# Kernel optimization log

Hardware: AMD Instinct MI355X
Metric: run time of the kernel (lower is better)

Reference implementation:

```python
import jax, jax.numpy as jnp
import numpy as np

STATE_DIM = 2048
OBS_DIM = 512
STEPS = 8192
PROC_STD = 0.1 ** 0.5   # sqrt(process_noise_var)
OBS_STD = 0.5 ** 0.5    # sqrt(observation_noise_var)


def setup_inputs() -> dict:
    key = jax.random.key(0)
    k1, k2, k3, k4, k5 = jax.random.split(key, 5)
    initial_state = jax.random.normal(k1, (STATE_DIM,), dtype=jnp.float32)
    process_noise = jax.random.normal(k2, (STEPS, STATE_DIM), dtype=jnp.float32)
    obs_noise = jax.random.normal(k3, (STEPS, OBS_DIM), dtype=jnp.float32)
    # Near-stable transition matrix (torch default is exactly identity, which is
    # marginally stable; keep spectral radius < 1 for an 8192-step rollout).
    A = 0.99 * jnp.eye(STATE_DIM, dtype=jnp.float32) \
        + 1e-4 * jax.random.normal(k4, (STATE_DIM, STATE_DIM), dtype=jnp.float32)
    C = 0.02 * jax.random.normal(k5, (OBS_DIM, STATE_DIM), dtype=jnp.float32)
    return {
        "initial_state": initial_state,
        "A": A,
        "C": C,
        "process_noise": process_noise,
        "obs_noise": obs_noise,
        "steps": STEPS,
    }


def reference(initial_state, A, C, process_noise, obs_noise, steps):
    # obs_t   = C @ state_t + obs_noise_t   * sqrt(obs_var)
    # state_{t+1} = A @ state_t + proc_noise_t * sqrt(proc_var)
    def step(state, noises):
        pn, on = noises
        obs = C @ state + on * OBS_STD
        new_state = A @ state + pn * PROC_STD
        return new_state, obs

    _, observations = jax.lax.scan(step, initial_state, (process_noise, obs_noise))
    return observations  # (steps, obs_dim)
```

## Files before the change

### kernel.cpp

```cpp
#include <hip/hip_runtime.h>


#define SD 2048
#define OD 512
#define NT 8192
#define BLK 64
#define KB 128
#define KBP (KB+16)
#define NP 7
#define NPH 6
#define NPN 5
#define PROC_STD 0.31622776601683794f
#define OBS_STD  0.7071067811865476f

typedef __attribute__((ext_vector_type(8))) short v8s;
typedef __attribute__((ext_vector_type(4))) float v4f;

__device__ __forceinline__ unsigned short f2bf(float f) {
    union { float f; unsigned int u; } v; v.f = f;
    unsigned int r = v.u + 0x7fffu + ((v.u >> 16) & 1u);
    return (unsigned short)(r >> 16);
}
__device__ __forceinline__ float bf2f(unsigned short u) {
    union { unsigned int ui; float f; } cv; cv.ui = (unsigned int)u << 16;
    return cv.f;
}

#define GLD16(g, l) __builtin_amdgcn_global_load_lds( \
    (const __attribute__((address_space(1))) unsigned int*)(g), \
    (__attribute__((address_space(3))) unsigned int*)(l), 16, 0, 0)


__device__ __forceinline__ void body_g64(unsigned short* SH,
        const unsigned short* __restrict__ A,
        const unsigned short* __restrict__ B, int ldb,
        int tM, int tN, int mode,
        unsigned short* __restrict__ obf, int ldo,
        float* __restrict__ o32,
        const unsigned short* __restrict__ X1,
        const unsigned short* __restrict__ X2,
        float c1, float c2) {
    unsigned short* Al = SH;
    unsigned short* Xt = SH + 64 * 40;
    int tid = threadIdx.x, lane = tid & 63, w = tid >> 6;
    int m16 = lane & 15, q = lane >> 4;
    int ar = tid >> 2, ao = (tid & 3) * 8;
    int xk = tid >> 3, xn = (tid & 7) * 8;
    int qb = xk >> 3;
    v4f acc[4] = {{0,0,0,0},{0,0,0,0},{0,0,0,0},{0,0,0,0}};

    v8s av = *(const v8s*)(A + (size_t)(tM + ar) * SD + ao);
    v8s xv = *(const v8s*)(B + (size_t)xk * ldb + tN + xn);
    for (int k0 = 0; k0 < SD; k0 += 32) {
        *(v8s*)(Al + ar * 40 + ao) = av;
#pragma unroll
        for (int c = 0; c < 8; ++c) {
            int n = xn + c, sw = (n >> 3) & 3;
            Xt[n * 40 + (((qb ^ sw) << 3) | (xk & 7))] = xv[c];
        }
        __syncthreads();
        if (k0 + 32 < SD) {
            av = *(const v8s*)(A + (size_t)(tM + ar) * SD + (k0 + 32) + ao);
            xv = *(const v8s*)(B + (size_t)(k0 + 32 + xk) * ldb + tN + xn);
        }
        v8s a = *(const v8s*)(Al + (w * 16 + m16) * 40 + q * 8);
#pragma unroll
        for (int c = 0; c < 4; ++c) {
            int nl = c * 16 + m16, swn = (nl >> 3) & 3;
            v8s b = *(const v8s*)(Xt + nl * 40 + ((q ^ swn) << 3));
            acc[c] = __builtin_amdgcn_mfma_f32_16x16x32_bf16(a, b, acc[c], 0, 0, 0);
        }
        __syncthreads();
    }
#pragma unroll
    for (int c = 0; c < 4; ++c)
#pragma unroll
        for (int j = 0; j < 4; ++j) {
            int r = tM + w * 16 + q * 4 + j;
            int col = tN + c * 16 + m16;
            float v = acc[c][j];
            if (mode == 2) {
                size_t iS = (size_t)r * SD + col;
                v += o32[iS] + c1 * bf2f(X1[iS]) + c2 * bf2f(X2[iS]);
                o32[iS] = v;
                obf[iS] = f2bf(v);
            } else if (mode == 3) {
                size_t iS = (size_t)r * SD + col;
                v = c1 * o32[iS] + v;
                o32[iS] = v;
                obf[iS] = f2bf(v);
            } else if (mode == 1) {
                o32[(size_t)r * ldo + col] = v;
            } else {
                obf[(size_t)r * ldo + col] = f2bf(v);
            }
        }
}

__device__ __forceinline__ void body_horner(unsigned short* SH, int bx,
        const unsigned short* __restrict__ Abf,
        const unsigned short* __restrict__ Xbf,
        const float* __restrict__ Wp,
        float* __restrict__ X32o,
        unsigned short* __restrict__ Xbfo) {
    unsigned short* Al = SH;
    unsigned short* Xt = SH + 32 * 72;
    int tM = (bx & 63) * 32, tN = (bx >> 6) * 32;
    int tid = threadIdx.x, lane = tid & 63, w = tid >> 6;
    int m16 = lane & 15, q = lane >> 4;
    int ar = tid >> 3, ao = (tid & 7) * 8;
    int xk = tid >> 2, xn = (tid & 3) * 8;
    int qb = xk >> 3;
    v4f acc = {0, 0, 0, 0};
    v8s av = *(const v8s*)(Abf + (size_t)(tM + ar) * SD + ao);
    v8s xv = *(const v8s*)(Xbf + (size_t)xk * KB + tN + xn);
    int nl = (w & 1) * 16 + m16;
    int swn = (nl >> 3) & 3;
    int rl = (w >> 1) * 16 + m16;
    for (int k0 = 0; k0 < SD; k0 += 64) {
        *(v8s*)(Al + ar * 72 + ao) = av;
#pragma unroll
        for (int c = 0; c < 8; ++c) {
            int n = xn + c, sw = (n >> 3) & 3;
            Xt[n * 72 + (((qb ^ sw) << 3) | (xk & 7))] = xv[c];
        }
        __syncthreads();
        if (k0 + 64 < SD) {
            av = *(const v8s*)(Abf + (size_t)(tM + ar) * SD + (k0 + 64) + ao);
            xv = *(const v8s*)(Xbf + (size_t)(k0 + 64 + xk) * KB + tN + xn);
        }
#pragma unroll
        for (int ch = 0; ch < 2; ++ch) {
            v8s a = *(const v8s*)(Al + rl * 72 + ch * 32 + q * 8);
            int q2 = ch * 4 + q;
            v8s b = *(const v8s*)(Xt + nl * 72 + ((q2 ^ swn) << 3));
            acc = __builtin_amdgcn_mfma_f32_16x16x32_bf16(a, b, acc, 0, 0, 0);
        }
        __syncthreads();
    }
#pragma unroll
    for (int j = 0; j < 4; ++j) {
        int r = tM + (w >> 1) * 16 + q * 4 + j;
        int kc = tN + (w & 1) * 16 + m16;
        int idx = r * KB + kc;
        float v = acc[j] + Wp[idx];
        X32o[idx] = v;
        if (Xbfo) Xbfo[idx] = f2bf(v);
    }
}

__device__ __forceinline__ void body_scan(unsigned short* SH, int bx,
        const unsigned short* __restrict__ Mrbf,
        const unsigned short* __restrict__ Sbf_in,
        const float* __restrict__ S32_in,
        float* __restrict__ S32_out,
        unsigned short* __restrict__ Sbf_out,
        float ar, int shift) {
    unsigned short* Al = SH;
    unsigned short* Xt = SH + 32 * 72;
    int tM = (bx & 63) * 32, tN = (bx >> 6) * 32;
    int tid = threadIdx.x, lane = tid & 63, w = tid >> 6;
    int m16 = lane & 15, q = lane >> 4;
    int ar_ = tid >> 3, ao = (tid & 7) * 8;
    int xk = tid >> 2, xn = (tid & 3) * 8;
    int qb = xk >> 3;
    int coff = tN + xn + 16 - shift;
    v4f acc = {0, 0, 0, 0};
    v8s av = *(const v8s*)(Mrbf + (size_t)(tM + ar_) * SD + ao);
    v8s xv = *(const v8s*)(Sbf_in + (size_t)xk * KBP + coff);
    int nl = (w & 1) * 16 + m16;
    int swn = (nl >> 3) & 3;
    int rl = (w >> 1) * 16 + m16;
    for (int k0 = 0; k0 < SD; k0 += 64) {
        *(v8s*)(Al + ar_ * 72 + ao) = av;
#pragma unroll
        for (int c = 0; c < 8; ++c) {
            int n = xn + c, sw = (n >> 3) & 3;
            Xt[n * 72 + (((qb ^ sw) << 3) | (xk & 7))] = xv[c];
        }
        __syncthreads();
        if (k0 + 64 < SD) {
            av = *(const v8s*)(Mrbf + (size_t)(tM + ar_) * SD + (k0 + 64) + ao);
            xv = *(const v8s*)(Sbf_in + (size_t)(k0 + 64 + xk) * KBP + coff);
        }
#pragma unroll
        for (int ch = 0; ch < 2; ++ch) {
            v8s a = *(const v8s*)(Al + rl * 72 + ch * 32 + q * 8);
            int q2 = ch * 4 + q;
            v8s b = *(const v8s*)(Xt + nl * 72 + ((q2 ^ swn) << 3));
            acc = __builtin_amdgcn_mfma_f32_16x16x32_bf16(a, b, acc, 0, 0, 0);
        }
        __syncthreads();
    }
#pragma unroll
    for (int j = 0; j < 4; ++j) {
        int r = tM + (w >> 1) * 16 + q * 4 + j;
        int kc = tN + (w & 1) * 16 + m16;
        int idx = r * KB + kc;
        int ksh = kc - shift;
        float v = S32_in[idx] + acc[j] + (ksh >= 0 ? ar * S32_in[r * KB + ksh] : 0.f);
        S32_out[idx] = v;
        Sbf_out[(size_t)r * KBP + kc + 16] = f2bf(v);
    }
}

__device__ __forceinline__ void body_g128(unsigned short* SH, int bid,
        const unsigned short* __restrict__ Aptr, int lda,
        const unsigned short* __restrict__ Bptr, int ldb,
        int mtiles, int npx,
        unsigned short* __restrict__ obf, size_t ldo) {
    unsigned short* As = SH;
    unsigned short* Bs = SH + 4096;
    int tid = threadIdx.x, lane = tid & 63, w = tid >> 6;
    int mT = (bid >> 3) % mtiles;
    int nT = (bid & 7) * npx + (bid >> 3) / mtiles;
    int tM = mT * 128, tN = nT * 128;
    int wr = w >> 1, wc = w & 1;
    int m16 = lane & 15, q = lane >> 4;
    int srow = lane >> 2, sk8 = lane & 3;
    const unsigned short* ga0 = Aptr + (size_t)(tM + w * 16 + srow) * lda + sk8 * 8;
    const unsigned short* ga1 = ga0 + (size_t)64 * lda;
    const unsigned short* gb0 = Bptr + (size_t)(tN + w * 16 + srow) * ldb + sk8 * 8;
    const unsigned short* gb1 = gb0 + (size_t)64 * ldb;
    unsigned short* la0 = As + w * 512;
    unsigned short* la1 = As + 2048 + w * 512;
    unsigned short* lb0 = Bs + w * 512;
    unsigned short* lb1 = Bs + 2048 + w * 512;

    v4f acc[4][4];
#pragma unroll
    for (int mi = 0; mi < 4; ++mi)
#pragma unroll
        for (int ni = 0; ni < 4; ++ni) acc[mi][ni] = (v4f){0, 0, 0, 0};

    GLD16(ga0, la0); GLD16(ga1, la1); GLD16(gb0, lb0); GLD16(gb1, lb1);
    ga0 += 32; ga1 += 32; gb0 += 32; gb1 += 32;
    __syncthreads();

    int arow = (wr * 64 + m16) * 32 + q * 8;
    int brow = (wc * 64 + m16) * 32 + q * 8;
    for (int k0 = 0; k0 < SD; k0 += 32) {
        v8s a[4], b[4];
#pragma unroll
        for (int mi = 0; mi < 4; ++mi) a[mi] = *(const v8s*)(As + arow + mi * 512);
#pragma unroll
        for (int ni = 0; ni < 4; ++ni) b[ni] = *(const v8s*)(Bs + brow + ni * 512);
        __syncthreads();
        if (k0 + 32 < SD) {
            GLD16(ga0, la0); GLD16(ga1, la1); GLD16(gb0, lb0); GLD16(gb1, lb1);
            ga0 += 32; ga1 += 32; gb0 += 32; gb1 += 32;
        }
#pragma unroll
        for (int mi = 0; mi < 4; ++mi)
#pragma unroll
            for (int ni = 0; ni < 4; ++ni)
                acc[mi][ni] = __builtin_amdgcn_mfma_f32_16x16x32_bf16(a[mi], b[ni],
                                                                      acc[mi][ni], 0, 0, 0);
        __syncthreads();
    }
#pragma unroll
    for (int mi = 0; mi < 4; ++mi)
#pragma unroll
        for (int ni = 0; ni < 4; ++ni)
#pragma unroll
            for (int j = 0; j < 4; ++j) {
                int row = tM + wr * 64 + mi * 16 + q * 4 + j;
                int col = tN + wc * 64 + ni * 16 + m16;
                obf[(size_t)row * ldo + col] = f2bf(acc[mi][ni][j]);
            }
}


__device__ double d_binom(int m, int p) {
    if (p < 0 || p > m) return 0.0;
    double c = 1.0;
    for (int q = 1; q <= p; ++q) c = c * (double)(m - p + q) / (double)q;
    return c;
}
__device__ double d_p99(int n) {
    double r = 1.0;
    for (int q = 0; q < n; ++q) r *= 0.99;
    return r;
}

__global__ __launch_bounds__(256) void k_prepAll(const float* __restrict__ A,
                                                 const float* __restrict__ C,
                                                 unsigned short* __restrict__ Ebf,
                                                 float* __restrict__ M, float c1,
                                                 unsigned short* __restrict__ Cbf,
                                                 float* __restrict__ wW,
                                                 float* __restrict__ cW,
                                                 unsigned short* __restrict__ Tbf) {
    int bid = blockIdx.x;
    if (bid < 16384) {
        int idx = bid * 256 + threadIdx.x;
        int r = idx >> 11, c = idx & 2047;
        float e = A[idx] - (r == c ? 0.99f : 0.0f);
        Ebf[idx] = f2bf(e);
        M[idx] = c1 * e;
    } else if (bid < 20480) {
        int idx = (bid - 16384) * 256 + threadIdx.x;
        Cbf[idx] = f2bf(C[idx]);
    } else {
        int idx = (bid - 20480) * 256 + threadIdx.x;
        if (idx < NP * 64) {
            int p = idx >> 6, j = idx & 63;
            int m = 63 - j;
            wW[idx] = (p <= m) ? (float)((double)PROC_STD * d_binom(m, p) * d_p99(m - p)) : 0.f;
            cW[idx] = (p <= j) ? (float)(d_binom(j, p) * d_p99(j - p)) : 0.f;
        }
        if (idx < NP * 64 * 64) {
            int p = idx >> 12, j = (idx >> 6) & 63, i = idx & 63;
            int mm = i - 1 - j;
            float t = (mm >= p) ? (float)((double)PROC_STD * d_binom(mm, p) * d_p99(mm - p)) : 0.f;
            Tbf[idx] = f2bf(t);
        }
    }
}

__global__ __launch_bounds__(256) void k_wsum(const float* __restrict__ pn,
                                              const float* __restrict__ wW,
                                              float* __restrict__ W32,
                                              unsigned short* __restrict__ Wbf,
                                              unsigned short* __restrict__ Vbf,
                                              unsigned short* __restrict__ pnbf) {
    __shared__ float ws[NP * 64];
    int tid = threadIdx.x;
    for (int t = tid; t < NP * 64; t += 256) ws[t] = wW[t];
    __syncthreads();
    int bx = blockIdx.x;
    int k = bx >> 1, dc = bx & 1;
    int d0 = dc * 1024 + tid * 4;
    float acc[NP][4];
#pragma unroll
    for (int p = 0; p < NP; ++p)
#pragma unroll
        for (int u = 0; u < 4; ++u) acc[p][u] = 0.f;
    for (int j = 0; j < 64; ++j) {
        size_t gi = (size_t)(k * BLK + j) * SD + d0;
        float4 v = *(const float4*)(pn + gi);
        ushort4 b4;
        b4.x = f2bf(v.x); b4.y = f2bf(v.y); b4.z = f2bf(v.z); b4.w = f2bf(v.w);
        *(ushort4*)(pnbf + gi) = b4;
#pragma unroll
        for (int p = 0; p < NP; ++p) {
            float wv = ws[p * 64 + j];
            acc[p][0] += wv * v.x; acc[p][1] += wv * v.y;
            acc[p][2] += wv * v.z; acc[p][3] += wv * v.w;
        }
    }
#pragma unroll
    for (int jj = 0; jj < 3; ++jj)
#pragma unroll
        for (int u = 0; u < 4; ++u) {
            W32[((size_t)jj * SD + d0 + u) * KB + k] = acc[2 * jj][u];
            Wbf[((size_t)jj * SD + d0 + u) * KB + k] = f2bf(acc[2 * jj + 1][u]);
        }
#pragma unroll
    for (int u = 0; u < 4; ++u)
        Vbf[(size_t)(d0 + u) * KB + k] = f2bf(acc[6][u]);
}

__global__ __launch_bounds__(256) void k_combP(const unsigned short* __restrict__ Ebf,
                                               const unsigned short* __restrict__ E2,
                                               const unsigned short* __restrict__ E3,
                                               unsigned short* __restrict__ P,
                                               float c4, float c5, float c6) {
    int idx = blockIdx.x * 256 + threadIdx.x;
    P[idx] = f2bf(c4 * bf2f(Ebf[idx]) + c5 * bf2f(E2[idx]) + c6 * bf2f(E3[idx]));
}

__global__ __launch_bounds__(256) void k_nn_ce(const unsigned short* __restrict__ L,
                                               const unsigned short* __restrict__ X,
                                               unsigned short* __restrict__ NNout,
                                               const unsigned short* __restrict__ CEa,
                                               const unsigned short* __restrict__ CEb,
                                               unsigned short* __restrict__ CEout) {
    __shared__ __align__(16) unsigned short SH[5120];
    int bid = blockIdx.x;
    if (bid < 1024)
        body_g64(SH, L, X, SD, (bid & 31) * 64, (bid >> 5) * 64, 0, NNout, SD,
                 nullptr, nullptr, nullptr, 0.f, 0.f);
    else {
        int bx = bid - 1024;
        body_g64(SH, CEa, CEb, SD, (bx & 7) * 64, (bx >> 3) * 64, 0, CEout, SD,
                 nullptr, nullptr, nullptr, 0.f, 0.f);
    }
}

__global__ __launch_bounds__(256) void k_M_Y(const unsigned short* __restrict__ E3,
                                             const unsigned short* __restrict__ P,
                                             float* __restrict__ M32,
                                             const unsigned short* __restrict__ E2,
                                             unsigned short* __restrict__ Mbf,
                                             float c2, float c3,
                                             const unsigned short* __restrict__ Ebf,
                                             const unsigned short* __restrict__ Wbf,
                                             const float* __restrict__ W32,
                                             float* __restrict__ Y32) {
    __shared__ __align__(16) unsigned short SH[5120];
    int bid = blockIdx.x;
    if (bid < 1024)
        body_g64(SH, E3, P, SD, (bid & 31) * 64, (bid >> 5) * 64, 2, Mbf, SD,
                 M32, E2, E3, c2, c3);
    else {
        int l = bid - 1024;
        int j = l >> 8, bx = l & 255;
        body_horner(SH, bx, Ebf, Wbf + (size_t)j * SD * KB, W32 + (size_t)j * SD * KB,
                    Y32 + (size_t)j * SD * KB, nullptr);
    }
}

__global__ __launch_bounds__(256) void k_ce2_z(const unsigned short* __restrict__ CEall,
                                               const unsigned short* __restrict__ E2,
                                               const float* __restrict__ Y32,
                                               const unsigned short* __restrict__ Vbf0,
                                               float* __restrict__ V32o,
                                               unsigned short* __restrict__ Vbfo) {
    __shared__ __align__(16) unsigned short SH[5120];
    int bid = blockIdx.x;
    if (bid < 512) {
        int y = bid >> 8, bx = bid & 255;
        body_g64(SH, CEall + (size_t)(1 + y) * OD * SD, E2, SD,
                 (bx & 7) * 64, (bx >> 3) * 64, 0,
                 (unsigned short*)(CEall + (size_t)(3 + y) * OD * SD), SD,
                 nullptr, nullptr, nullptr, 0.f, 0.f);
    } else
        body_horner(SH, bid - 512, E2, Vbf0, Y32 + (size_t)2 * SD * KB, V32o, Vbfo);
}

__global__ __launch_bounds__(256) void k_ce1_z(const unsigned short* __restrict__ CEall,
                                               const unsigned short* __restrict__ E2,
                                               const float* __restrict__ Y32,
                                               const unsigned short* __restrict__ Vbf1,
                                               float* __restrict__ V32o,
                                               unsigned short* __restrict__ Vbfo) {
    __shared__ __align__(16) unsigned short SH[5120];
    int bid = blockIdx.x;
    if (bid < 256)
        body_g64(SH, CEall + (size_t)3 * OD * SD, E2, SD,
                 (bid & 7) * 64, (bid >> 3) * 64, 0,
                 (unsigned short*)(CEall + (size_t)5 * OD * SD), SD,
                 nullptr, nullptr, nullptr, 0.f, 0.f);
    else
        body_horner(SH, bid - 256, E2, Vbf1, Y32 + (size_t)SD * KB, V32o, Vbfo);
}

__global__ __launch_bounds__(256) void k_hornerZ(const unsigned short* __restrict__ E2,
                                                 const unsigned short* __restrict__ Vbf0,
                                                 const float* __restrict__ Y32,
                                                 float* __restrict__ V32o) {
    __shared__ __align__(16) unsigned short SH[5120];
    body_horner(SH, blockIdx.x, E2, Vbf0, Y32, V32o, nullptr);
}

__global__ __launch_bounds__(256) void k_scan_init(const float* __restrict__ s0,
                                                   const float* __restrict__ U,
                                                   float* __restrict__ S32,
                                                   unsigned short* __restrict__ Sbf0,
                                                   unsigned short* __restrict__ Sbf1) {
    int idx = blockIdx.x * 256 + threadIdx.x;
    int d = idx / KBP, c = idx - d * KBP;
    if (c < 16) { Sbf0[idx] = 0; Sbf1[idx] = 0; return; }
    int k = c - 16;
    float v = (k == 0) ? s0[d] : U[(size_t)d * KB + (k - 1)];
    S32[(size_t)d * KB + k] = v;
    Sbf0[idx] = f2bf(v);
}

__global__ __launch_bounds__(256) void k_sqscan(const unsigned short* __restrict__ Lbf,
                                                float* __restrict__ M32,
                                                unsigned short* __restrict__ Mbfo,
                                                float twoa,
                                                const unsigned short* __restrict__ Sbf_in,
                                                const float* __restrict__ S32_in,
                                                float* __restrict__ S32_out,
                                                unsigned short* __restrict__ Sbf_out,
                                                float ar, int shift) {
    __shared__ __align__(16) unsigned short SH[5120];
    int bid = blockIdx.x;
    if (bid < 1024)
        body_g64(SH, Lbf, Lbf, SD, (bid & 31) * 64, (bid >> 5) * 64, 3, Mbfo, SD,
                 M32, nullptr, nullptr, twoa, 0.f);
    else
        body_scan(SH, bid - 1024, Lbf, Sbf_in, S32_in, S32_out, Sbf_out, ar, shift);
}

__global__ __launch_bounds__(256) void k_scan3(const unsigned short* __restrict__ Mrbf,
                                               const unsigned short* __restrict__ Sbf_in,
                                               const float* __restrict__ S32_in,
                                               float* __restrict__ S32_out,
                                               unsigned short* __restrict__ Sbf_out,
                                               float ar, int shift) {
    __shared__ __align__(16) unsigned short SH[5120];
    body_scan(SH, blockIdx.x, Mrbf, Sbf_in, S32_in, S32_out, Sbf_out, ar, shift);
}

__global__ __launch_bounds__(256) void k_scan16(const float* __restrict__ S32_in,
                                                float* __restrict__ S32_out,
                                                unsigned short* __restrict__ Sbf_out,
                                                float a4) {
    int idx = blockIdx.x * 256 + threadIdx.x;
    int d = idx >> 7, k = idx & 127;
    float v = S32_in[idx] + (k >= 16 ? a4 * S32_in[idx - 16] : 0.f);
    S32_out[idx] = v;
    Sbf_out[(size_t)d * KBP + k + 16] = f2bf(v);
}

__global__ __launch_bounds__(256) void k_pall_h(const unsigned short* __restrict__ CEall,
                                                const unsigned short* __restrict__ pnbf,
                                                unsigned short* __restrict__ Pall,
                                                const unsigned short* __restrict__ Sbf16,
                                                float* __restrict__ H) {
    __shared__ __align__(16) unsigned short SH[8192];
    int bid = blockIdx.x;
    if (bid < 1280)
        body_g128(SH, bid, CEall, SD, pnbf, SD, 20, 8, Pall, (size_t)NT);
    else {
        int l = bid - 1280;
        int y = l >> 4, bx = l & 15;
        body_g64(SH, CEall + (size_t)y * OD * SD, Sbf16, KBP,
                 (bx & 7) * 64, (bx >> 3) * 64, 1, nullptr, KB,
                 H + (size_t)y * OD * KB, nullptr, nullptr, 0.f, 0.f);
    }
}

__global__ __launch_bounds__(256) void k_final2(const unsigned short* __restrict__ P,
                                                const unsigned short* __restrict__ Tbf,
                                                const float* __restrict__ H,
                                                const float* __restrict__ cW,
                                                const float* __restrict__ on,
                                                float* __restrict__ out) {
    __shared__ __align__(16) float obsT[64][65];
    unsigned short* Al = (unsigned short*)obsT;
    unsigned short* Xt = Al + 64 * 40;
    int bx = blockIdx.x;
    int kb = bx >> 3, ob = bx & 7;
    int o0 = ob * 64;
    int tid = threadIdx.x, lane = tid & 63, w = tid >> 6;
    int m16 = lane & 15, q = lane >> 4;
    int ar = tid >> 2, ao = (tid & 3) * 8;
    int xk = tid >> 3, xn = (tid & 7) * 8;
    int qb = xk >> 3;
    v4f acc[4] = {{0,0,0,0},{0,0,0,0},{0,0,0,0},{0,0,0,0}};
    const unsigned short* Abase = P + (size_t)kb * 64;

    v8s av = *(const v8s*)(Abase + (size_t)(o0 + ar) * NT + ao);
    v8s xv = *(const v8s*)(Tbf + xk * 64 + xn);
    for (int kc = 0; kc < 2 * NPN; ++kc) {
        *(v8s*)(Al + ar * 40 + ao) = av;
#pragma unroll
        for (int c = 0; c < 8; ++c) {
            int n = xn + c, sw = (n >> 3) & 3;
            Xt[n * 40 + (((qb ^ sw) << 3) | (xk & 7))] = xv[c];
        }
        __syncthreads();
        if (kc + 1 < 2 * NPN) {
            int p = (kc + 1) >> 1, j0 = ((kc + 1) & 1) * 32;
            av = *(const v8s*)(Abase + (size_t)(p * OD + o0 + ar) * NT + j0 + ao);
            xv = *(const v8s*)(Tbf + p * 4096 + (j0 + xk) * 64 + xn);
        }
        v8s a = *(const v8s*)(Al + (w * 16 + m16) * 40 + q * 8);
#pragma unroll
        for (int c = 0; c < 4; ++c) {
            int nl = c * 16 + m16, swn = (nl >> 3) & 3;
            v8s b = *(const v8s*)(Xt + nl * 40 + ((q ^ swn) << 3));
            acc[c] = __builtin_amdgcn_mfma_f32_16x16x32_bf16(a, b, acc[c], 0, 0, 0);
        }
        __syncthreads();
    }
#pragma unroll
    for (int c = 0; c < 4; ++c)
#pragma unroll
        for (int j = 0; j < 4; ++j)
            obsT[w * 16 + q * 4 + j][c * 16 + m16] = acc[c][j];
    __syncthreads();
    int g = tid >> 6;
    float Hv[NPH];
#pragma unroll
    for (int p = 0; p < NPH; ++p)
        Hv[p] = H[((size_t)p * OD + o0 + lane) * KB + kb];
#pragma unroll
    for (int r = 0; r < 16; ++r) {
        int trow = r * 4 + g;
        float a2 = obsT[lane][trow];
#pragma unroll
        for (int p = 0; p < NPH; ++p) a2 += cW[p * 64 + trow] * Hv[p];
        size_t oidx = (size_t)(kb * 64 + trow) * OD + o0 + lane;
        out[oidx] = a2 + OBS_STD * on[oidx];
    }
}

extern "C" void kernel_launch(void* const* d_in, const int* in_sizes, int n_in,
                              void* d_out, int out_size, void* d_ws, size_t ws_size,
                              hipStream_t stream) {
    const float* s0 = (const float*)d_in[0];
    const float* A  = (const float*)d_in[1];
    const float* C  = (const float*)d_in[2];
    const float* pn = (const float*)d_in[3];
    const float* on = (const float*)d_in[4];
    float* out = (float*)d_out;

    char* p = (char*)d_ws;
    auto take = [&](size_t n) { char* r = p; p += (n + 255) & ~(size_t)255; return r; };
    unsigned short* Ebf = (unsigned short*)take((size_t)SD * SD * 2);
    unsigned short* CEall = (unsigned short*)take((size_t)NPH * OD * SD * 2);
    float* M            = (float*)take((size_t)SD * SD * 4);
    unsigned short* Xp0 = (unsigned short*)take((size_t)SD * SD * 2);
    unsigned short* Xp1 = (unsigned short*)take((size_t)SD * SD * 2);
    unsigned short* Xp2 = (unsigned short*)take((size_t)SD * SD * 2);
    unsigned short* Pall = (unsigned short*)M;
    unsigned short* Mbf = (unsigned short*)take((size_t)SD * SD * 2);
    float* W32          = (float*)take((size_t)3 * SD * KB * 4);
    unsigned short* Wbf = (unsigned short*)take((size_t)3 * SD * KB * 2);
    float* Y32          = (float*)take((size_t)3 * SD * KB * 4);
    float* V32[2] = {(float*)take((size_t)SD * KB * 4), (float*)take((size_t)SD * KB * 4)};
    unsigned short* Vbf[2] = {(unsigned short*)take((size_t)SD * KB * 2),
                              (unsigned short*)take((size_t)SD * KB * 2)};
    float* SC32[2] = {(float*)take((size_t)SD * KB * 4), (float*)take((size_t)SD * KB * 4)};
    unsigned short* SCbf[2] = {(unsigned short*)take((size_t)SD * KBP * 2),
                               (unsigned short*)take((size_t)SD * KBP * 2)};
    float* wW   = (float*)take((size_t)NP * 64 * 4);
    float* cW   = (float*)take((size_t)NP * 64 * 4);
    unsigned short* Tbf = (unsigned short*)take((size_t)NP * 64 * 64 * 2);
    unsigned short* pnbf = (unsigned short*)take((size_t)SD * NT * 2);
    float* H    = (float*)take((size_t)NPH * OD * KB * 4);

    double pw[65]; pw[0] = 1.0;
    for (int m = 1; m <= 64; ++m) pw[m] = pw[m - 1] * 0.99;
    const double bin[7] = {1, 64, 2016, 41664, 635376, 7624512, 74974368};
    float cf[7];
    for (int m = 1; m <= 6; ++m) cf[m] = (float)(bin[m] * pw[64 - m]);
    float a64 = (float)pw[64];

    k_prepAll<<<20592, 256, 0, stream>>>(A, C, Ebf, M, cf[1], CEall, wW, cW, Tbf);
    k_wsum<<<256, 256, 0, stream>>>(pn, wW, W32, Wbf, Vbf[0], pnbf);
    k_nn_ce<<<1280, 256, 0, stream>>>(Ebf, Ebf, Xp0, CEall, Ebf, CEall + (size_t)OD * SD);
    k_nn_ce<<<1280, 256, 0, stream>>>(Ebf, Xp0, Xp1, CEall, Xp0, CEall + (size_t)2 * OD * SD);
    k_combP<<<SD * SD / 256, 256, 0, stream>>>(Ebf, Xp0, Xp1, Xp2, cf[4], cf[5], cf[6]);
    k_M_Y<<<1792, 256, 0, stream>>>(Xp1, Xp2, M, Xp0, Mbf, cf[2], cf[3], Ebf, Wbf, W32, Y32);
    k_ce2_z<<<768, 256, 0, stream>>>(CEall, Xp0, Y32, Vbf[0], V32[1], Vbf[1]);
    k_ce1_z<<<512, 256, 0, stream>>>(CEall, Xp0, Y32, Vbf[1], V32[0], Vbf[0]);
    k_hornerZ<<<256, 256, 0, stream>>>(Xp0, Vbf[0], Y32, V32[1]);
    k_scan_init<<<SD * KBP / 256, 256, 0, stream>>>(s0, V32[1], SC32[0], SCbf[0], SCbf[1]);
    float a = a64;
    k_sqscan<<<1280, 256, 0, stream>>>(Mbf, M, Xp0, 2.f * a,
                                       SCbf[0], SC32[0], SC32[1], SCbf[1], a, 1);
    a *= a;
    k_sqscan<<<1280, 256, 0, stream>>>(Xp0, M, Mbf, 2.f * a,
                                       SCbf[1], SC32[1], SC32[0], SCbf[0], a, 2);
    a *= a;
    k_sqscan<<<1280, 256, 0, stream>>>(Mbf, M, Xp0, 2.f * a,
                                       SCbf[0], SC32[0], SC32[1], SCbf[1], a, 4);
    a *= a;
    k_scan3<<<256, 256, 0, stream>>>(Xp0, SCbf[1], SC32[1], SC32[0], SCbf[0], a, 8);
    a *= a;
    k_scan16<<<SD * KB / 256, 256, 0, stream>>>(SC32[0], SC32[1], SCbf[1], a);
    k_pall_h<<<1376, 256, 0, stream>>>(CEall, pnbf, Pall, SCbf[1] + 16, H);
    k_final2<<<1024, 256, 0, stream>>>(Pall, Tbf, H, cW, on, out);
}
```

Baseline: 787.8 us.

## Fuse small elementwise kernels into GEMM epilogues and drop fp32 M copy

Removes the fp32 M matrix: the squaring epilogues now read the bf16 previous operand instead of fp32 state, and k_prepAll no longer writes M. Folds the combP polynomial into the second nn GEMM epilogue (mode 4) and the scan-init into the Horner kernel. Co-schedules the scan3 step with the Pall GEMM and applies the last scan16 shift algebraically inside k_final2 on G. This cuts kernel launches and the memory traffic of several full 2048x2048 passes, at the cost of lower precision in the M recurrence (bf16 instead of fp32 accumulation).

```diff
diff --git a/kernel.cpp b/kernel.cpp
--- a/kernel.cpp
+++ b/kernel.cpp
@@ -39,7 +39,9 @@
         float* __restrict__ o32,
         const unsigned short* __restrict__ X1,
         const unsigned short* __restrict__ X2,
-        float c1, float c2) {
+        const unsigned short* __restrict__ X3,
+        unsigned short* __restrict__ Pout,
+        float c1, float c2, float c3) {
     unsigned short* Al = SH;
     unsigned short* Xt = SH + 64 * 40;
     int tid = threadIdx.x, lane = tid & 63, w = tid >> 6;
@@ -79,16 +81,16 @@
             int r = tM + w * 16 + q * 4 + j;
             int col = tN + c * 16 + m16;
             float v = acc[c][j];
+            size_t iS = (size_t)r * SD + col;
             if (mode == 2) {
-                size_t iS = (size_t)r * SD + col;
-                v += o32[iS] + c1 * bf2f(X1[iS]) + c2 * bf2f(X2[iS]);
-                o32[iS] = v;
+                v += c1 * bf2f(X1[iS]) + c2 * bf2f(X2[iS]) + c3 * bf2f(X3[iS]);
                 obf[iS] = f2bf(v);
             } else if (mode == 3) {
-                size_t iS = (size_t)r * SD + col;
-                v = c1 * o32[iS] + v;
-                o32[iS] = v;
+                v = c1 * bf2f(X1[iS]) + v;
                 obf[iS] = f2bf(v);
+            } else if (mode == 4) {
+                obf[iS] = f2bf(v);
+                Pout[iS] = f2bf(c1 * bf2f(X1[iS]) + c2 * bf2f(X2[iS]) + c3 * v);
             } else if (mode == 1) {
                 o32[(size_t)r * ldo + col] = v;
             } else {
@@ -102,7 +104,8 @@
         const unsigned short* __restrict__ Xbf,
         const float* __restrict__ Wp,
         float* __restrict__ X32o,
-        unsigned short* __restrict__ Xbfo) {
+        unsigned short* __restrict__ Xbfo,
+        int initShift) {
     unsigned short* Al = SH;
     unsigned short* Xt = SH + 32 * 72;
     int tM = (bx & 63) * 32, tN = (bx >> 6) * 32;
@@ -142,10 +145,16 @@
     for (int j = 0; j < 4; ++j) {
         int r = tM + (w >> 1) * 16 + q * 4 + j;
         int kc = tN + (w & 1) * 16 + m16;
-        int idx = r * KB + kc;
-        float v = acc[j] + Wp[idx];
-        X32o[idx] = v;
-        if (Xbfo) Xbfo[idx] = f2bf(v);
+        float v = acc[j] + Wp[r * KB + kc];
+        if (initShift) {
+            if (kc < 127) {
+                X32o[r * KB + kc + 1] = v;
+                Xbfo[(size_t)r * KBP + kc + 17] = f2bf(v);
+            }
+        } else {
+            X32o[r * KB + kc] = v;
+            if (Xbfo) Xbfo[r * KB + kc] = f2bf(v);
+        }
     }
 }
 
@@ -286,7 +295,6 @@
 __global__ __launch_bounds__(256) void k_prepAll(const float* __restrict__ A,
                                                  const float* __restrict__ C,
                                                  unsigned short* __restrict__ Ebf,
-                                                 float* __restrict__ M, float c1,
                                                  unsigned short* __restrict__ Cbf,
                                                  float* __restrict__ wW,
                                                  float* __restrict__ cW,
@@ -297,7 +305,6 @@
         int r = idx >> 11, c = idx & 2047;
         float e = A[idx] - (r == c ? 0.99f : 0.0f);
         Ebf[idx] = f2bf(e);
-        M[idx] = c1 * e;
     } else if (bid < 20480) {
         int idx = (bid - 16384) * 256 + threadIdx.x;
         Cbf[idx] = f2bf(C[idx]);
@@ -361,40 +368,35 @@
         Vbf[(size_t)(d0 + u) * KB + k] = f2bf(acc[6][u]);
 }
 
-__global__ __launch_bounds__(256) void k_combP(const unsigned short* __restrict__ Ebf,
-                                               const unsigned short* __restrict__ E2,
-                                               const unsigned short* __restrict__ E3,
-                                               unsigned short* __restrict__ P,
-                                               float c4, float c5, float c6) {
-    int idx = blockIdx.x * 256 + threadIdx.x;
-    P[idx] = f2bf(c4 * bf2f(Ebf[idx]) + c5 * bf2f(E2[idx]) + c6 * bf2f(E3[idx]));
-}
-
 __global__ __launch_bounds__(256) void k_nn_ce(const unsigned short* __restrict__ L,
                                                const unsigned short* __restrict__ X,
                                                unsigned short* __restrict__ NNout,
                                                const unsigned short* __restrict__ CEa,
                                                const unsigned short* __restrict__ CEb,
-                                               unsigned short* __restrict__ CEout) {
+                                               unsigned short* __restrict__ CEout,
+                                               int mode,
+                                               unsigned short* __restrict__ Pout,
+                                               const unsigned short* __restrict__ X1,
+                                               const unsigned short* __restrict__ X2,
+                                               float c1, float c2, float c3) {
     __shared__ __align__(16) unsigned short SH[5120];
     int bid = blockIdx.x;
     if (bid < 1024)
-        body_g64(SH, L, X, SD, (bid & 31) * 64, (bid >> 5) * 64, 0, NNout, SD,
-                 nullptr, nullptr, nullptr, 0.f, 0.f);
+        body_g64(SH, L, X, SD, (bid & 31) * 64, (bid >> 5) * 64, mode, NNout, SD,
+                 nullptr, X1, X2, nullptr, Pout, c1, c2, c3);
     else {
         int bx = bid - 1024;
         body_g64(SH, CEa, CEb, SD, (bx & 7) * 64, (bx >> 3) * 64, 0, CEout, SD,
-                 nullptr, nullptr, nullptr, 0.f, 0.f);
+                 nullptr, nullptr, nullptr, nullptr, nullptr, 0.f, 0.f, 0.f);
     }
 }
 
 __global__ __launch_bounds__(256) void k_M_Y(const unsigned short* __restrict__ E3,
                                              const unsigned short* __restrict__ P,
-                                             float* __restrict__ M32,
+                                             const unsigned short* __restrict__ Ebf,
                                              const unsigned short* __restrict__ E2,
                                              unsigned short* __restrict__ Mbf,
-                                             float c2, float c3,
-                                             const unsigned short* __restrict__ Ebf,
+                                             float c1, float c2, float c3,
                                              const unsigned short* __restrict__ Wbf,
                                              const float* __restrict__ W32,
                                              float* __restrict__ Y32) {
@@ -402,12 +404,12 @@
     int bid = blockIdx.x;
     if (bid < 1024)
         body_g64(SH, E3, P, SD, (bid & 31) * 64, (bid >> 5) * 64, 2, Mbf, SD,
-                 M32, E2, E3, c2, c3);
+                 nullptr, Ebf, E2, E3, nullptr, c1, c2, c3);
     else {
         int l = bid - 1024;
         int j = l >> 8, bx = l & 255;
         body_horner(SH, bx, Ebf, Wbf + (size_t)j * SD * KB, W32 + (size_t)j * SD * KB,
-                    Y32 + (size_t)j * SD * KB, nullptr);
+                    Y32 + (size_t)j * SD * KB, nullptr, 0);
     }
 }
 
@@ -424,9 +426,9 @@
         body_g64(SH, CEall + (size_t)(1 + y) * OD * SD, E2, SD,
                  (bx & 7) * 64, (bx >> 3) * 64, 0,
                  (unsigned short*)(CEall + (size_t)(3 + y) * OD * SD), SD,
-                 nullptr, nullptr, nullptr, 0.f, 0.f);
+                 nullptr, nullptr, nullptr, nullptr, nullptr, 0.f, 0.f, 0.f);
     } else
-        body_horner(SH, bid - 512, E2, Vbf0, Y32 + (size_t)2 * SD * KB, V32o, Vbfo);
+        body_horner(SH, bid - 512, E2, Vbf0, Y32 + (size_t)2 * SD * KB, V32o, Vbfo, 0);
 }
 
 __global__ __launch_bounds__(256) void k_ce1_z(const unsigned short* __restrict__ CEall,
@@ -441,35 +443,36 @@
         body_g64(SH, CEall + (size_t)3 * OD * SD, E2, SD,
                  (bid & 7) * 64, (bid >> 3) * 64, 0,
                  (unsigned short*)(CEall + (size_t)5 * OD * SD), SD,
-                 nullptr, nullptr, nullptr, 0.f, 0.f);
+                 nullptr, nullptr, nullptr, nullptr, nullptr, 0.f, 0.f, 0.f);
     else
-        body_horner(SH, bid - 256, E2, Vbf1, Y32 + (size_t)SD * KB, V32o, Vbfo);
-}
-
-__global__ __launch_bounds__(256) void k_hornerZ(const unsigned short* __restrict__ E2,
-                                                 const unsigned short* __restrict__ Vbf0,
-                                                 const float* __restrict__ Y32,
-                                                 float* __restrict__ V32o) {
+        body_horner(SH, bid - 256, E2, Vbf1, Y32 + (size_t)SD * KB, V32o, Vbfo, 0);
+}
+
+__global__ __launch_bounds__(256) void k_hornerZI(const unsigned short* __restrict__ E2,
+                                                  const unsigned short* __restrict__ Vbf0,
+                                                  const float* __restrict__ Y32,
+                                                  const float* __restrict__ s0,
+                                                  float* __restrict__ S32,
+                                                  unsigned short* __restrict__ Sbf0,
+                                                  unsigned short* __restrict__ Sbf1) {
     __shared__ __align__(16) unsigned short SH[5120];
-    body_horner(SH, blockIdx.x, E2, Vbf0, Y32, V32o, nullptr);
-}
-
-__global__ __launch_bounds__(256) void k_scan_init(const float* __restrict__ s0,
-                                                   const float* __restrict__ U,
-                                                   float* __restrict__ S32,
-                                                   unsigned short* __restrict__ Sbf0,
-                                                   unsigned short* __restrict__ Sbf1) {
-    int idx = blockIdx.x * 256 + threadIdx.x;
-    int d = idx / KBP, c = idx - d * KBP;
-    if (c < 16) { Sbf0[idx] = 0; Sbf1[idx] = 0; return; }
-    int k = c - 16;
-    float v = (k == 0) ? s0[d] : U[(size_t)d * KB + (k - 1)];
-    S32[(size_t)d * KB + k] = v;
-    Sbf0[idx] = f2bf(v);
+    int bid = blockIdx.x;
+    if (bid < 256)
+        body_horner(SH, bid, E2, Vbf0, Y32, S32, Sbf0, 1);
+    else {
+        int idx = (bid - 256) * 256 + threadIdx.x;
+        int d = idx >> 4, c = idx & 15;
+        Sbf0[(size_t)d * KBP + c] = 0;
+        Sbf1[(size_t)d * KBP + c] = 0;
+        if (c == 0) {
+            float v = s0[d];
+            S32[d * KB] = v;
+            Sbf0[(size_t)d * KBP + 16] = f2bf(v);
+        }
+    }
 }
 
 __global__ __launch_bounds__(256) void k_sqscan(const unsigned short* __restrict__ Lbf,
-                                                float* __restrict__ M32,
                                                 unsigned short* __restrict__ Mbfo,
                                                 float twoa,
                                                 const unsigned short* __restrict__ Sbf_in,
@@ -481,56 +484,45 @@
     int bid = blockIdx.x;
     if (bid < 1024)
         body_g64(SH, Lbf, Lbf, SD, (bid & 31) * 64, (bid >> 5) * 64, 3, Mbfo, SD,
-                 M32, nullptr, nullptr, twoa, 0.f);
+                 nullptr, Lbf, nullptr, nullptr, nullptr, twoa, 0.f, 0.f);
     else
         body_scan(SH, bid - 1024, Lbf, Sbf_in, S32_in, S32_out, Sbf_out, ar, shift);
 }
 
-__global__ __launch_bounds__(256) void k_scan3(const unsigned short* __restrict__ Mrbf,
-                                               const unsigned short* __restrict__ Sbf_in,
-                                               const float* __restrict__ S32_in,
-                                               float* __restrict__ S32_out,
-                                               unsigned short* __restrict__ Sbf_out,
-                                               float ar, int shift) {
-    __shared__ __align__(16) unsigned short SH[5120];
-    body_scan(SH, blockIdx.x, Mrbf, Sbf_in, S32_in, S32_out, Sbf_out, ar, shift);
-}
-
-__global__ __launch_bounds__(256) void k_scan16(const float* __restrict__ S32_in,
+__global__ __launch_bounds__(256) void k_pall_s(const unsigned short* __restrict__ CEall,
+                                                const unsigned short* __restrict__ pnbf,
+                                                unsigned short* __restrict__ Pall,
+                                                const unsigned short* __restrict__ M4,
+                                                const unsigned short* __restrict__ Sbf_in,
+                                                const float* __restrict__ S32_in,
                                                 float* __restrict__ S32_out,
                                                 unsigned short* __restrict__ Sbf_out,
-                                                float a4) {
-    int idx = blockIdx.x * 256 + threadIdx.x;
-    int d = idx >> 7, k = idx & 127;
-    float v = S32_in[idx] + (k >= 16 ? a4 * S32_in[idx - 16] : 0.f);
-    S32_out[idx] = v;
-    Sbf_out[(size_t)d * KBP + k + 16] = f2bf(v);
-}
-
-__global__ __launch_bounds__(256) void k_pall_h(const unsigned short* __restrict__ CEall,
-                                                const unsigned short* __restrict__ pnbf,
-                                                unsigned short* __restrict__ Pall,
-                                                const unsigned short* __restrict__ Sbf16,
-                                                float* __restrict__ H) {
+                                                float ar) {
     __shared__ __align__(16) unsigned short SH[8192];
     int bid = blockIdx.x;
     if (bid < 1280)
         body_g128(SH, bid, CEall, SD, pnbf, SD, 20, 8, Pall, (size_t)NT);
-    else {
-        int l = bid - 1280;
-        int y = l >> 4, bx = l & 15;
-        body_g64(SH, CEall + (size_t)y * OD * SD, Sbf16, KBP,
-                 (bx & 7) * 64, (bx >> 3) * 64, 1, nullptr, KB,
-                 H + (size_t)y * OD * KB, nullptr, nullptr, 0.f, 0.f);
-    }
+    else
+        body_scan(SH, bid - 1280, M4, Sbf_in, S32_in, S32_out, Sbf_out, ar, 8);
+}
+
+__global__ __launch_bounds__(256) void k_G(const unsigned short* __restrict__ CEall,
+                                           const unsigned short* __restrict__ Sbf16,
+                                           float* __restrict__ G) {
+    __shared__ __align__(16) unsigned short SH[5120];
+    int l = blockIdx.x;
+    int y = l >> 4, bx = l & 15;
+    body_g64(SH, CEall + (size_t)y * OD * SD, Sbf16, KBP,
+             (bx & 7) * 64, (bx >> 3) * 64, 1, nullptr, KB,
+             G + (size_t)y * OD * KB, nullptr, nullptr, nullptr, nullptr, 0.f, 0.f, 0.f);
 }
 
 __global__ __launch_bounds__(256) void k_final2(const unsigned short* __restrict__ P,
                                                 const unsigned short* __restrict__ Tbf,
-                                                const float* __restrict__ H,
+                                                const float* __restrict__ G,
                                                 const float* __restrict__ cW,
                                                 const float* __restrict__ on,
-                                                float* __restrict__ out) {
+                                                float* __restrict__ out, float af) {
     __shared__ __align__(16) float obsT[64][65];
     unsigned short* Al = (unsigned short*)obsT;
     unsigned short* Xt = Al + 64 * 40;
@@ -578,8 +570,10 @@
     int g = tid >> 6;
     float Hv[NPH];
 #pragma unroll
-    for (int p = 0; p < NPH; ++p)
-        Hv[p] = H[((size_t)p * OD + o0 + lane) * KB + kb];
+    for (int p = 0; p < NPH; ++p) {
+        size_t base = ((size_t)p * OD + o0 + lane) * KB + kb;
+        Hv[p] = G[base] + (kb >= 16 ? af * G[base - 16] : 0.f);
+    }
 #pragma unroll
     for (int r = 0; r < 16; ++r) {
         int trow = r * 4 + g;
@@ -605,11 +599,10 @@
     auto take = [&](size_t n) { char* r = p; p += (n + 255) & ~(size_t)255; return r; };
     unsigned short* Ebf = (unsigned short*)take((size_t)SD * SD * 2);
     unsigned short* CEall = (unsigned short*)take((size_t)NPH * OD * SD * 2);
-    float* M            = (float*)take((size_t)SD * SD * 4);
+    unsigned short* Pall = (unsigned short*)take((size_t)(NPN * OD) * NT * 2);
     unsigned short* Xp0 = (unsigned short*)take((size_t)SD * SD * 2);
     unsigned short* Xp1 = (unsigned short*)take((size_t)SD * SD * 2);
     unsigned short* Xp2 = (unsigned short*)take((size_t)SD * SD * 2);
-    unsigned short* Pall = (unsigned short*)M;
     unsigned short* Mbf = (unsigned short*)take((size_t)SD * SD * 2);
     float* W32          = (float*)take((size_t)3 * SD * KB * 4);
     unsigned short* Wbf = (unsigned short*)take((size_t)3 * SD * KB * 2);
@@ -624,7 +617,7 @@
     float* cW   = (float*)take((size_t)NP * 64 * 4);
     unsigned short* Tbf = (unsigned short*)take((size_t)NP * 64 * 64 * 2);
     unsigned short* pnbf = (unsigned short*)take((size_t)SD * NT * 2);
-    float* H    = (float*)take((size_t)NPH * OD * KB * 4);
+    float* G    = (float*)take((size_t)NPH * OD * KB * 4);
 
     double pw[65]; pw[0] = 1.0;
     for (int m = 1; m <= 64; ++m) pw[m] = pw[m - 1] * 0.99;
@@ -633,29 +626,31 @@
     for (int m = 1; m <= 6; ++m) cf[m] = (float)(bin[m] * pw[64 - m]);
     float a64 = (float)pw[64];
 
-    k_prepAll<<<20592, 256, 0, stream>>>(A, C, Ebf, M, cf[1], CEall, wW, cW, Tbf);
+    k_prepAll<<<20592, 256, 0, stream>>>(A, C, Ebf, CEall, wW, cW, Tbf);
     k_wsum<<<256, 256, 0, stream>>>(pn, wW, W32, Wbf, Vbf[0], pnbf);
-    k_nn_ce<<<1280, 256, 0, stream>>>(Ebf, Ebf, Xp0, CEall, Ebf, CEall + (size_t)OD * SD);
-    k_nn_ce<<<1280, 256, 0, stream>>>(Ebf, Xp0, Xp1, CEall, Xp0, CEall + (size_t)2 * OD * SD);
-    k_combP<<<SD * SD / 256, 256, 0, stream>>>(Ebf, Xp0, Xp1, Xp2, cf[4], cf[5], cf[6]);
-    k_M_Y<<<1792, 256, 0, stream>>>(Xp1, Xp2, M, Xp0, Mbf, cf[2], cf[3], Ebf, Wbf, W32, Y32);
+    k_nn_ce<<<1280, 256, 0, stream>>>(Ebf, Ebf, Xp0, CEall, Ebf, CEall + (size_t)OD * SD,
+                                      0, nullptr, nullptr, nullptr, 0.f, 0.f, 0.f);
+    k_nn_ce<<<1280, 256, 0, stream>>>(Ebf, Xp0, Xp1, CEall, Xp0,
+                                      CEall + (size_t)2 * OD * SD,
+                                      4, Xp2, Ebf, Xp0, cf[4], cf[5], cf[6]);
+    k_M_Y<<<1792, 256, 0, stream>>>(Xp1, Xp2, Ebf, Xp0, Mbf, cf[1], cf[2], cf[3],
+                                    Wbf, W32, Y32);
     k_ce2_z<<<768, 256, 0, stream>>>(CEall, Xp0, Y32, Vbf[0], V32[1], Vbf[1]);
     k_ce1_z<<<512, 256, 0, stream>>>(CEall, Xp0, Y32, Vbf[1], V32[0], Vbf[0]);
-    k_hornerZ<<<256, 256, 0, stream>>>(Xp0, Vbf[0], Y32, V32[1]);
-    k_scan_init<<<SD * KBP / 256, 256, 0, stream>>>(s0, V32[1], SC32[0], SCbf[0], SCbf[1]);
+    k_hornerZI<<<384, 256, 0, stream>>>(Xp0, Vbf[0], Y32, s0, SC32[0], SCbf[0], SCbf[1]);
     float a = a64;
-    k_sqscan<<<1280, 256, 0, stream>>>(Mbf, M, Xp0, 2.f * a,
+    k_sqscan<<<1280, 256, 0, stream>>>(Mbf, Xp0, 2.f * a,
                                        SCbf[0], SC32[0], SC32[1], SCbf[1], a, 1);
     a *= a;
-    k_sqscan<<<1280, 256, 0, stream>>>(Xp0, M, Mbf, 2.f * a,
+    k_sqscan<<<1280, 256, 0, stream>>>(Xp0, Xp1, 2.f * a,
                                        SCbf[1], SC32[1], SC32[0], SCbf[0], a, 2);
     a *= a;
-    k_sqscan<<<1280, 256, 0, stream>>>(Mbf, M, Xp0, 2.f * a,
+    k_sqscan<<<1280, 256, 0, stream>>>(Xp1, Xp0, 2.f * a,
                                        SCbf[0], SC32[0], SC32[1], SCbf[1], a, 4);
     a *= a;
-    k_scan3<<<256, 256, 0, stream>>>(Xp0, SCbf[1], SC32[1], SC32[0], SCbf[0], a, 8);
+    k_pall_s<<<1536, 256, 0, stream>>>(CEall, pnbf, Pall, Xp0,
+                                       SCbf[1], SC32[1], SC32[0], SCbf[0], a);
     a *= a;
-    k_scan16<<<SD * KB / 256, 256, 0, stream>>>(SC32[0], SC32[1], SCbf[1], a);
-    k_pall_h<<<1376, 256, 0, stream>>>(CEall, pnbf, Pall, SCbf[1] + 16, H);
-    k_final2<<<1024, 256, 0, stream>>>(Pall, Tbf, H, cW, on, out);
-}
+    k_G<<<96, 256, 0, stream>>>(CEall, SCbf[0] + 16, G);
+    k_final2<<<1024, 256, 0, stream>>>(Pall, Tbf, G, cW, on, out, a);
+}
```

Result: faster. 760.1 us (-3.5%).
